# Optimization experiments

Hardware: AMD Instinct MI355X
Metric: run time of the kernel (lower is better)

## Reference

```python
import jax, jax.numpy as jnp
import numpy as np

B, T, C = 2, 2048, 768
H = 12
D = C // H  # head size = 64
F = 4 * C
EPS = 1e-5


def _layernorm(x, g, b):
    mu = jnp.mean(x, axis=-1, keepdims=True)
    var = jnp.var(x, axis=-1, keepdims=True)
    return (x - mu) * jax.lax.rsqrt(var + EPS) * g + b


def setup_inputs() -> dict:
    key = jax.random.key(0)
    ks = jax.random.split(key, 16)
    s_in = 1.0 / np.sqrt(C)
    s_ff = 1.0 / np.sqrt(F)
    return {
        "x": jax.random.normal(ks[0], (B, T, C), dtype=jnp.float32),
        # per-head projection weights, stacked [H, C, D] (no bias, as in nn.Linear(bias=False))
        "Wq": jax.random.uniform(ks[1], (H, C, D), jnp.float32, -s_in, s_in),
        "Wk": jax.random.uniform(ks[2], (H, C, D), jnp.float32, -s_in, s_in),
        "Wv": jax.random.uniform(ks[3], (H, C, D), jnp.float32, -s_in, s_in),
        "Wp": jax.random.uniform(ks[4], (C, C), jnp.float32, -s_in, s_in),
        "bp": jax.random.uniform(ks[5], (C,), jnp.float32, -s_in, s_in),
        "W1": jax.random.uniform(ks[6], (C, F), jnp.float32, -s_in, s_in),
        "b1": jax.random.uniform(ks[7], (F,), jnp.float32, -s_in, s_in),
        "W2": jax.random.uniform(ks[8], (F, C), jnp.float32, -s_ff, s_ff),
        "b2": jax.random.uniform(ks[9], (C,), jnp.float32, -s_ff, s_ff),
        "ln1_g": jnp.ones((C,), jnp.float32),
        "ln1_b": jnp.zeros((C,), jnp.float32),
        "ln2_g": jnp.ones((C,), jnp.float32),
        "ln2_b": jnp.zeros((C,), jnp.float32),
    }


def reference(x, Wq, Wk, Wv, Wp, bp, W1, b1, W2, b2, ln1_g, ln1_b, ln2_g, ln2_b):
    # --- self-attention sublayer (pre-LN) ---
    h = _layernorm(x, ln1_g, ln1_b)                      # [B,T,C]
    q = jnp.einsum('btc,hcd->bhtd', h, Wq)
    k = jnp.einsum('btc,hcd->bhtd', h, Wk)
    v = jnp.einsum('btc,hcd->bhtd', h, Wv)
    # NOTE: original scales by C**-0.5 where C = n_embd (full width), not head size
    scale = C ** (-0.5)
    wei = jnp.einsum('bhtd,bhsd->bhts', q, k) * scale    # [B,H,T,T]
    causal = jnp.tril(jnp.ones((T, T), dtype=bool))
    wei = jnp.where(causal, wei, -jnp.inf)
    wei = jax.nn.softmax(wei, axis=-1)
    out = jnp.einsum('bhts,bhsd->bhtd', wei, v)          # [B,H,T,D]
    out = out.transpose(0, 2, 1, 3).reshape(B, T, C)     # concat heads
    sa = out @ Wp + bp
    x = x + sa
    # --- feed-forward sublayer (pre-LN); ReLU after BOTH linears, as in source ---
    h2 = _layernorm(x, ln2_g, ln2_b)
    ff = jax.nn.relu(jax.nn.relu(h2 @ W1 + b1) @ W2 + b2)
    return x + ff
```

## Files before the change

kernel.cpp:

```cpp
#include <hip/hip_runtime.h>
#include <hip/hip_bf16.h>

#define TSEQ 2048
#define CDIM 768
#define NHEAD 12
#define DHEAD 64
#define FDIM 3072
#define MROWS 4096
#define BH 24

typedef __attribute__((ext_vector_type(8))) short short8;
typedef __attribute__((ext_vector_type(4))) float f32x4;

__device__ inline unsigned short f2bf(float f) {
  __hip_bfloat16 h = __float2bfloat16(f);
  return __builtin_bit_cast(unsigned short, h);
}
__device__ inline float bf2f(unsigned short u) {
  unsigned int v = ((unsigned int)u) << 16;
  return __builtin_bit_cast(float, v);
}

__device__ inline void gload16(const unsigned short* g, unsigned short* l) {
  __builtin_amdgcn_global_load_lds(
      (const __attribute__((address_space(1))) unsigned int*)g,
      (__attribute__((address_space(3))) unsigned int*)l, 16, 0, 0);
}

__global__ __launch_bounds__(256) void prep_all(
    const float* __restrict__ Wq, const float* __restrict__ Wk,
    const float* __restrict__ Wv, const float* __restrict__ Wp,
    const float* __restrict__ W1, const float* __restrict__ W2,
    unsigned short* __restrict__ WqkvT, unsigned short* __restrict__ WpT,
    unsigned short* __restrict__ W1T, unsigned short* __restrict__ W2T,
    const float* __restrict__ x, const float* __restrict__ ln1g,
    const float* __restrict__ ln1b, unsigned short* __restrict__ h1) {
  __shared__ float tile[32][33];
  __shared__ float red[8];
  int b = blockIdx.x;
  if (b >= 6912) {
    int row = b - 6912;
    int tid = threadIdx.x;
    const float* xr = x + (size_t)row * CDIM;
    float v[3];
    float s = 0.f;
#pragma unroll
    for (int i = 0; i < 3; ++i) { v[i] = xr[tid + i * 256]; s += v[i]; }
#pragma unroll
    for (int m = 1; m < 64; m <<= 1) s += __shfl_xor(s, m);
    int w = tid >> 6;
    if ((tid & 63) == 0) red[w] = s;
    __syncthreads();
    float mean = (red[0] + red[1] + red[2] + red[3]) * (1.f / CDIM);
    float vs = 0.f;
#pragma unroll
    for (int i = 0; i < 3; ++i) { float d = v[i] - mean; vs += d * d; }
#pragma unroll
    for (int m = 1; m < 64; m <<= 1) vs += __shfl_xor(vs, m);
    if ((tid & 63) == 0) red[4 + w] = vs;
    __syncthreads();
    float var = (red[4] + red[5] + red[6] + red[7]) * (1.f / CDIM);
    float rstd = rsqrtf(var + 1e-5f);
    unsigned short* orow = h1 + (size_t)row * CDIM;
#pragma unroll
    for (int i = 0; i < 3; ++i) {
      int c = tid + i * 256;
      orow[c] = f2bf((v[i] - mean) * rstd * ln1g[c] + ln1b[c]);
    }
    return;
  }
  int xx = threadIdx.x & 31, y = threadIdx.x >> 5;
  if (b < 1728) {
    int cx = b % 24, dy = (b / 24) % 2, ph = b / 48;
    int proj = ph / NHEAD, h = ph % NHEAD;
    const float* in = (proj == 0 ? Wq : (proj == 1 ? Wk : Wv)) + (size_t)h * CDIM * DHEAD;
    int c0 = cx * 32, d0 = dy * 32;
#pragma unroll
    for (int i = 0; i < 4; ++i)
      tile[y + i * 8][xx] = in[(size_t)(c0 + y + i * 8) * DHEAD + d0 + xx];
    __syncthreads();
#pragma unroll
    for (int i = 0; i < 4; ++i)
      WqkvT[(size_t)(proj * CDIM + h * DHEAD + d0 + y + i * 8) * CDIM + c0 + xx] =
          f2bf(tile[xx][y + i * 8]);
  } else {
    const float* in;
    unsigned short* out;
    int R, C, bx, by;
    if (b < 2304) {
      int b2 = b - 1728;
      in = Wp; out = WpT; R = CDIM; C = CDIM; bx = b2 % 24; by = b2 / 24;
    } else if (b < 4608) {
      int b2 = b - 2304;
      in = W1; out = W1T; R = CDIM; C = FDIM; bx = b2 % 96; by = b2 / 96;
    } else {
      int b2 = b - 4608;
      in = W2; out = W2T; R = FDIM; C = CDIM; bx = b2 % 24; by = b2 / 24;
    }
    int c0 = bx * 32, r0 = by * 32;
#pragma unroll
    for (int i = 0; i < 4; ++i)
      tile[y + i * 8][xx] = in[(size_t)(r0 + y + i * 8) * C + c0 + xx];
    __syncthreads();
#pragma unroll
    for (int i = 0; i < 4; ++i)
      out[(size_t)(c0 + y + i * 8) * R + r0 + xx] = f2bf(tile[xx][y + i * 8]);
  }
}

__global__ __launch_bounds__(256) void ln_kernel(
    const float* __restrict__ x, const float* __restrict__ g,
    const float* __restrict__ b, unsigned short* __restrict__ out) {
  int row = blockIdx.x;
  int tid = threadIdx.x;
  const float* xr = x + (size_t)row * CDIM;
  float v[3];
  float s = 0.f;
#pragma unroll
  for (int i = 0; i < 3; ++i) { v[i] = xr[tid + i * 256]; s += v[i]; }
#pragma unroll
  for (int m = 1; m < 64; m <<= 1) s += __shfl_xor(s, m);
  __shared__ float red[8];
  int w = tid >> 6;
  if ((tid & 63) == 0) red[w] = s;
  __syncthreads();
  float mean = (red[0] + red[1] + red[2] + red[3]) * (1.f / CDIM);
  float vs = 0.f;
#pragma unroll
  for (int i = 0; i < 3; ++i) { float d = v[i] - mean; vs += d * d; }
#pragma unroll
  for (int m = 1; m < 64; m <<= 1) vs += __shfl_xor(vs, m);
  if ((tid & 63) == 0) red[4 + w] = vs;
  __syncthreads();
  float var = (red[4] + red[5] + red[6] + red[7]) * (1.f / CDIM);
  float rstd = rsqrtf(var + 1e-5f);
  unsigned short* orow = out + (size_t)row * CDIM;
#pragma unroll
  for (int i = 0; i < 3; ++i) {
    int c = tid + i * 256;
    orow[c] = f2bf((v[i] - mean) * rstd * g[c] + b[c]);
  }
}

template <int EPI, int SPLITK = 1>
__global__ __launch_bounds__(256) void gemm_bt(
    const unsigned short* __restrict__ A, const unsigned short* __restrict__ BT,
    int M, int N, int K,
    const float* __restrict__ bias, const float* __restrict__ aux,
    float* __restrict__ outf, unsigned short* __restrict__ outb,
    unsigned short* __restrict__ qo, unsigned short* __restrict__ ko,
    unsigned short* __restrict__ vo) {
  __shared__ unsigned short As[128 * 64];
  __shared__ unsigned short Bs[128 * 64];
  int tid = threadIdx.x;
  int lane = tid & 63, wave = tid >> 6;
  int wr = wave >> 1, wc = wave & 1;
  int l15 = lane & 15, lg = lane >> 4;
  int lr = lane >> 3, lc = lane & 7;
  int chunk = gridDim.x >> 3;
  int logical = (blockIdx.x & 7) * chunk + (blockIdx.x >> 3);
  int mt = M >> 7;
  int tiles = mt * (N >> 7);
  int split = logical / tiles;
  int tl = logical % tiles;
  size_t bm = (size_t)(tl % mt) * 128, bn = (size_t)(tl / mt) * 128;
  int Ks = K / SPLITK;
  int kbeg = split * Ks, kend = kbeg + Ks;
  f32x4 acc[4][4] = {};

  for (int kt = kbeg; kt < kend; kt += 64) {
#pragma unroll
    for (int i = 0; i < 4; ++i) {
      int r0 = (wave * 4 + i) * 8;
      gload16(A + (bm + r0 + lr) * K + kt + (lc ^ lr) * 8, &As[r0 * 64]);
      gload16(BT + (bn + r0 + lr) * K + kt + (lc ^ lr) * 8, &Bs[r0 * 64]);
    }
    __syncthreads();
    __builtin_amdgcn_s_setprio(1);
#pragma unroll
    for (int kk = 0; kk < 64; kk += 32) {
      int kb = kk + lg * 8;
      short8 af[4], bfr[4];
#pragma unroll
      for (int m = 0; m < 4; ++m) {
        int row = wr * 64 + m * 16 + l15;
        af[m] = *reinterpret_cast<const short8*>(&As[row * 64 + (kb ^ ((row & 7) << 3))]);
      }
#pragma unroll
      for (int n = 0; n < 4; ++n) {
        int row = wc * 64 + n * 16 + l15;
        bfr[n] = *reinterpret_cast<const short8*>(&Bs[row * 64 + (kb ^ ((row & 7) << 3))]);
      }
#pragma unroll
      for (int m = 0; m < 4; ++m)
#pragma unroll
        for (int n = 0; n < 4; ++n)
          acc[m][n] = __builtin_amdgcn_mfma_f32_16x16x32_bf16(af[m], bfr[n], acc[m][n], 0, 0, 0);
    }
    __builtin_amdgcn_s_setprio(0);
    __syncthreads();
  }

#pragma unroll
  for (int m = 0; m < 4; ++m) {
#pragma unroll
    for (int n = 0; n < 4; ++n) {
#pragma unroll
      for (int r = 0; r < 4; ++r) {
        int row = (int)bm + wr * 64 + m * 16 + lg * 4 + r;
        int col = (int)bn + wc * 64 + n * 16 + l15;
        float val = acc[m][n][r];
        if constexpr (EPI == 0) {
          int proj = col / CDIM, rem = col % CDIM;
          int h = rem >> 6, d = rem & 63;
          int b = row >> 11, t = row & (TSEQ - 1);
          if (proj == 0) {
            qo[(((size_t)(b * NHEAD + h)) * TSEQ + t) * DHEAD + d] =
                f2bf(val * 0.05205877247186126f);
          } else if (proj == 1) {
            ko[(((size_t)(b * NHEAD + h)) * TSEQ + t) * DHEAD + d] = f2bf(val);
          } else {
            vo[(((size_t)(b * NHEAD + h)) * DHEAD + d) * TSEQ + t] = f2bf(val);
          }
        } else if constexpr (EPI == 1) {
          size_t idx = (size_t)row * CDIM + col;
          outf[idx] = val + bias[col] + aux[idx];
        } else if constexpr (EPI == 2) {
          size_t idx = (size_t)row * FDIM + col;
          outb[idx] = f2bf(fmaxf(val + bias[col], 0.f));
        } else if constexpr (EPI == 3) {
          size_t idx = (size_t)row * CDIM + col;
          outf[idx] = aux[idx] + fmaxf(val + bias[col], 0.f);
        } else {
          outb[(size_t)split * M * N + (size_t)row * N + col] = f2bf(val);
        }
      }
    }
  }
}

__global__ __launch_bounds__(256) void ff2_reduce(
    const unsigned short* __restrict__ part,
    const float* __restrict__ bias, const float* __restrict__ x1,
    float* __restrict__ out) {
  int e = (blockIdx.x * 256 + threadIdx.x) * 4;
  int col = e % CDIM;
  float4 xv = *reinterpret_cast<const float4*>(x1 + e);
  float4 bv = *reinterpret_cast<const float4*>(bias + col);
  float s0 = 0.f, s1 = 0.f, s2 = 0.f, s3 = 0.f;
#pragma unroll
  for (int p = 0; p < 4; ++p) {
    short4 pv = *reinterpret_cast<const short4*>(part + (size_t)p * MROWS * CDIM + e);
    s0 += bf2f((unsigned short)pv.x);
    s1 += bf2f((unsigned short)pv.y);
    s2 += bf2f((unsigned short)pv.z);
    s3 += bf2f((unsigned short)pv.w);
  }
  float4 ov;
  ov.x = xv.x + fmaxf(s0 + bv.x, 0.f);
  ov.y = xv.y + fmaxf(s1 + bv.y, 0.f);
  ov.z = xv.z + fmaxf(s2 + bv.z, 0.f);
  ov.w = xv.w + fmaxf(s3 + bv.w, 0.f);
  *reinterpret_cast<float4*>(out + e) = ov;
}

__global__ __launch_bounds__(256) void attn_kernel(
    const unsigned short* __restrict__ Q, const unsigned short* __restrict__ Kd,
    const unsigned short* __restrict__ VT, unsigned short* __restrict__ O) {
  __shared__ unsigned short Kl[3][64 * 64];
  __shared__ unsigned short Vl[3][64 * 64];
  __shared__ unsigned short plds[4][16 * 64];
  int tid = threadIdx.x;
  int wave = tid >> 6, lane = tid & 63;
  int l15 = lane & 15, lg = lane >> 4;
  int bid = blockIdx.x;
  int xcd = bid & 7, idx = bid >> 3;
  int bh = xcd * 3 + idx / 16;
  int p = idx & 15;
  const unsigned short* qp = Q + (size_t)bh * TSEQ * DHEAD;
  const unsigned short* kp = Kd + (size_t)bh * TSEQ * DHEAD;
  const unsigned short* vp = VT + (size_t)bh * DHEAD * TSEQ;
  unsigned short* pw = plds[wave];
  int b = bh / NHEAD, h = bh % NHEAD;

  short8 ones;
  {
    unsigned short ov = (l15 == 0) ? (unsigned short)0x3F80 : (unsigned short)0;
#pragma unroll
    for (int j = 0; j < 8; ++j) ones[j] = (short)ov;
  }

  int lr = lane >> 3, lc = lane & 7;
  int jsw = lc ^ lr;

  auto stage = [&](int t, int buf) {
    int s0 = t * 64;
#pragma unroll
    for (int i = 0; i < 2; ++i) {
      int r0 = (wave * 2 + i) * 8;
      gload16(kp + (size_t)(s0 + r0 + lr) * DHEAD + jsw * 8, &Kl[buf][r0 * 64]);
      gload16(vp + (size_t)(r0 + lr) * TSEQ + s0 + jsw * 8, &Vl[buf][r0 * 64]);
    }
  };

  auto run_stripe = [&](int stripe) {
    int qbase = stripe * 64 + wave * 16;
    int nt = stripe + 1;
    short8 qf[2];
#pragma unroll
    for (int kk = 0; kk < 2; ++kk)
      qf[kk] = *reinterpret_cast<const short8*>(
          qp + (size_t)(qbase + l15) * DHEAD + kk * 32 + lg * 8);
    f32x4 oacc[5] = {};

    stage(0, 0);
    if (nt > 1) {
      stage(1, 1);
      asm volatile("s_waitcnt vmcnt(4)" ::: "memory");
    } else {
      asm volatile("s_waitcnt vmcnt(0)" ::: "memory");
    }
    __builtin_amdgcn_s_barrier();

    for (int t = 0; t < nt; ++t) {
      int cur = t % 3;
      bool pre2 = (t + 2 < nt);
      if (pre2) stage(t + 2, (t + 2) % 3);
      int s0 = t * 64;
      f32x4 sacc[4] = {};
      __builtin_amdgcn_s_setprio(1);
#pragma unroll
      for (int st = 0; st < 4; ++st) {
        int row = st * 16 + l15;
        int sw = row & 7;
#pragma unroll
        for (int kk = 0; kk < 2; ++kk) {
          short8 kf = *reinterpret_cast<const short8*>(
              &Kl[cur][row * 64 + (((kk * 4 + lg) ^ sw) * 8)]);
          sacc[st] = __builtin_amdgcn_mfma_f32_16x16x32_bf16(qf[kk], kf, sacc[st], 0, 0, 0);
        }
      }
      __builtin_amdgcn_s_setprio(0);
      bool last = (t == nt - 1);
#pragma unroll
      for (int r = 0; r < 4; ++r) {
        int qrow = qbase + lg * 4 + r;
        int prow = lg * 4 + r;
        int psw = (prow & 7) << 3;
        if (last) {
#pragma unroll
          for (int st = 0; st < 4; ++st) {
            float pv = exp2f(sacc[st][r]);
            if (s0 + st * 16 + l15 > qrow) pv = 0.f;
            pw[prow * 64 + ((st * 16 + l15) ^ psw)] = f2bf(pv);
          }
        } else {
#pragma unroll
          for (int st = 0; st < 4; ++st)
            pw[prow * 64 + ((st * 16 + l15) ^ psw)] = f2bf(exp2f(sacc[st][r]));
        }
      }
      int prsw = (l15 & 7) << 3;
      short8 pa0 = *reinterpret_cast<const short8*>(&pw[l15 * 64 + ((lg * 8) ^ prsw)]);
      short8 pa1 = *reinterpret_cast<const short8*>(&pw[l15 * 64 + ((32 + lg * 8) ^ prsw)]);
      __builtin_amdgcn_s_setprio(1);
#pragma unroll
      for (int n = 0; n < 4; ++n) {
        int row = n * 16 + l15;
        int sw = row & 7;
        short8 vf0 = *reinterpret_cast<const short8*>(&Vl[cur][row * 64 + ((lg ^ sw) * 8)]);
        oacc[n] = __builtin_amdgcn_mfma_f32_16x16x32_bf16(pa0, vf0, oacc[n], 0, 0, 0);
        short8 vf1 = *reinterpret_cast<const short8*>(&Vl[cur][row * 64 + (((4 + lg) ^ sw) * 8)]);
        oacc[n] = __builtin_amdgcn_mfma_f32_16x16x32_bf16(pa1, vf1, oacc[n], 0, 0, 0);
      }
      oacc[4] = __builtin_amdgcn_mfma_f32_16x16x32_bf16(pa0, ones, oacc[4], 0, 0, 0);
      oacc[4] = __builtin_amdgcn_mfma_f32_16x16x32_bf16(pa1, ones, oacc[4], 0, 0, 0);
      __builtin_amdgcn_s_setprio(0);
      if (pre2) asm volatile("s_waitcnt vmcnt(4)" ::: "memory");
      else      asm volatile("s_waitcnt vmcnt(0)" ::: "memory");
      __builtin_amdgcn_s_barrier();
    }

#pragma unroll
    for (int r = 0; r < 4; ++r) {
      float lsum = __shfl(oacc[4][r], lane & 48);
      float inv = 1.f / lsum;
      int row = qbase + lg * 4 + r;
#pragma unroll
      for (int n = 0; n < 4; ++n)
        O[(size_t)(b * TSEQ + row) * CDIM + h * DHEAD + n * 16 + l15] =
            f2bf(oacc[n][r] * inv);
    }
  };

  run_stripe(31 - p);
  run_stripe(p);
}

extern "C" void kernel_launch(void* const* d_in, const int* in_sizes, int n_in,
                              void* d_out, int out_size, void* d_ws, size_t ws_size,
                              hipStream_t stream) {
  const float* x    = (const float*)d_in[0];
  const float* Wq   = (const float*)d_in[1];
  const float* Wk   = (const float*)d_in[2];
  const float* Wv   = (const float*)d_in[3];
  const float* Wp   = (const float*)d_in[4];
  const float* bp   = (const float*)d_in[5];
  const float* W1   = (const float*)d_in[6];
  const float* b1   = (const float*)d_in[7];
  const float* W2   = (const float*)d_in[8];
  const float* b2   = (const float*)d_in[9];
  const float* ln1g = (const float*)d_in[10];
  const float* ln1b = (const float*)d_in[11];
  const float* ln2g = (const float*)d_in[12];
  const float* ln2b = (const float*)d_in[13];
  float* out = (float*)d_out;

  char* ws = (char*)d_ws;
  auto alloc = [&](size_t bytes) {
    char* p = ws;
    ws += (bytes + 255) & ~(size_t)255;
    return p;
  };
  unsigned short* h1    = (unsigned short*)alloc((size_t)MROWS * CDIM * 2);
  unsigned short* WqkvT = (unsigned short*)alloc((size_t)3 * CDIM * CDIM * 2);
  unsigned short* WpT   = (unsigned short*)alloc((size_t)CDIM * CDIM * 2);
  unsigned short* W1T   = (unsigned short*)alloc((size_t)FDIM * CDIM * 2);
  unsigned short* W2T   = (unsigned short*)alloc((size_t)CDIM * FDIM * 2);
  unsigned short* Qb    = (unsigned short*)alloc((size_t)BH * TSEQ * DHEAD * 2);
  unsigned short* Kb    = (unsigned short*)alloc((size_t)BH * TSEQ * DHEAD * 2);
  unsigned short* VTb   = (unsigned short*)alloc((size_t)BH * TSEQ * DHEAD * 2);
  unsigned short* AO    = (unsigned short*)alloc((size_t)MROWS * CDIM * 2);
  float*          x1    = (float*)alloc((size_t)MROWS * CDIM * 4);
  unsigned short* h2    = (unsigned short*)alloc((size_t)MROWS * CDIM * 2);
  unsigned short* a1    = (unsigned short*)alloc((size_t)MROWS * FDIM * 2);
  unsigned short* partF = Qb;

  prep_all<<<11008, 256, 0, stream>>>(Wq, Wk, Wv, Wp, W1, W2,
                                      WqkvT, WpT, W1T, W2T, x, ln1g, ln1b, h1);
  gemm_bt<0><<<576, 256, 0, stream>>>(h1, WqkvT, MROWS, 3 * CDIM, CDIM,
                                      nullptr, nullptr, nullptr, nullptr, Qb, Kb, VTb);
  attn_kernel<<<384, 256, 0, stream>>>(Qb, Kb, VTb, AO);
  gemm_bt<1><<<192, 256, 0, stream>>>(AO, WpT, MROWS, CDIM, CDIM,
                                      bp, x, x1, nullptr, nullptr, nullptr, nullptr);
  ln_kernel<<<4096, 256, 0, stream>>>(x1, ln2g, ln2b, h2);
  gemm_bt<2><<<768, 256, 0, stream>>>(h2, W1T, MROWS, FDIM, CDIM,
                                      b1, nullptr, nullptr, a1, nullptr, nullptr, nullptr);
  gemm_bt<4, 4><<<768, 256, 0, stream>>>(a1, W2T, MROWS, CDIM, FDIM,
                                         nullptr, nullptr, nullptr, partF,
                                         nullptr, nullptr, nullptr);
  ff2_reduce<<<3072, 256, 0, stream>>>(partF, b2, x1, out);
}
```

Before: 194.8 us.

## Stage V tile through LDS for coalesced transposed stores; split-K the output projection

The QKV GEMM epilogue now writes the V tiles into padded shared memory transposed and then emits 16-byte coalesced stores into the V^T layout, replacing scattered 2-byte strided stores. The output projection GEMM moves from 192 blocks with a fused residual epilogue to split-K=2 with 384 blocks, writing bf16 partials that a new templated reduce kernel sums with bias and residual. This targets the uncoalesced V write and the low occupancy of the small projection GEMM. The cost is an extra kernel launch, an extra round trip of partials through memory, and bf16 rounding of the partial sums.

```diff
diff --git a/kernel.cpp b/kernel.cpp
--- a/kernel.cpp
+++ b/kernel.cpp
@@ -150,8 +150,10 @@
     float* __restrict__ outf, unsigned short* __restrict__ outb,
     unsigned short* __restrict__ qo, unsigned short* __restrict__ ko,
     unsigned short* __restrict__ vo) {
-  __shared__ unsigned short As[128 * 64];
-  __shared__ unsigned short Bs[128 * 64];
+  constexpr int SH_CNT = (EPI == 0) ? 128 * 136 : 2 * 128 * 64;
+  __shared__ unsigned short sh[SH_CNT];
+  unsigned short* As = sh;
+  unsigned short* Bs = sh + 128 * 64;
   int tid = threadIdx.x;
   int lane = tid & 63, wave = tid >> 6;
   int wr = wave >> 1, wc = wave & 1;
@@ -201,55 +203,93 @@
     __syncthreads();
   }
 
-#pragma unroll
-  for (int m = 0; m < 4; ++m) {
-#pragma unroll
-    for (int n = 0; n < 4; ++n) {
-#pragma unroll
-      for (int r = 0; r < 4; ++r) {
-        int row = (int)bm + wr * 64 + m * 16 + lg * 4 + r;
-        int col = (int)bn + wc * 64 + n * 16 + l15;
-        float val = acc[m][n][r];
-        if constexpr (EPI == 0) {
-          int proj = col / CDIM, rem = col % CDIM;
-          int h = rem >> 6, d = rem & 63;
-          int b = row >> 11, t = row & (TSEQ - 1);
-          if (proj == 0) {
-            qo[(((size_t)(b * NHEAD + h)) * TSEQ + t) * DHEAD + d] =
-                f2bf(val * 0.05205877247186126f);
-          } else if (proj == 1) {
-            ko[(((size_t)(b * NHEAD + h)) * TSEQ + t) * DHEAD + d] = f2bf(val);
+  if constexpr (EPI == 0) {
+    if (bn >= 1536) {
+#pragma unroll
+      for (int m = 0; m < 4; ++m)
+#pragma unroll
+        for (int n = 0; n < 4; ++n)
+#pragma unroll
+          for (int r = 0; r < 4; ++r) {
+            int rowL = wr * 64 + m * 16 + lg * 4 + r;
+            int c = wc * 64 + n * 16 + l15;
+            sh[c * 136 + rowL] = f2bf(acc[m][n][r]);
+          }
+      __syncthreads();
+      int bb = (int)(bm >> 11);
+      int t0g = (int)(bm & 2047);
+      int vbase = (int)bn - 1536;
+#pragma unroll
+      for (int it = 0; it < 8; ++it) {
+        int ch = it * 256 + tid;
+        int c = ch >> 4, tlc = (ch & 15) * 8;
+        int vcol = vbase + c;
+        int hh = vcol >> 6, dd = vcol & 63;
+        *reinterpret_cast<int4*>(
+            vo + (((size_t)(bb * NHEAD + hh)) * DHEAD + dd) * TSEQ + t0g + tlc) =
+            *reinterpret_cast<const int4*>(&sh[c * 136 + tlc]);
+      }
+    } else {
+#pragma unroll
+      for (int m = 0; m < 4; ++m)
+#pragma unroll
+        for (int n = 0; n < 4; ++n)
+#pragma unroll
+          for (int r = 0; r < 4; ++r) {
+            int row = (int)bm + wr * 64 + m * 16 + lg * 4 + r;
+            int col = (int)bn + wc * 64 + n * 16 + l15;
+            float val = acc[m][n][r];
+            int proj = col / CDIM, rem = col % CDIM;
+            int h = rem >> 6, d = rem & 63;
+            int b = row >> 11, t = row & (TSEQ - 1);
+            if (proj == 0) {
+              qo[(((size_t)(b * NHEAD + h)) * TSEQ + t) * DHEAD + d] =
+                  f2bf(val * 0.05205877247186126f);
+            } else {
+              ko[(((size_t)(b * NHEAD + h)) * TSEQ + t) * DHEAD + d] = f2bf(val);
+            }
+          }
+    }
+  } else {
+#pragma unroll
+    for (int m = 0; m < 4; ++m) {
+#pragma unroll
+      for (int n = 0; n < 4; ++n) {
+#pragma unroll
+        for (int r = 0; r < 4; ++r) {
+          int row = (int)bm + wr * 64 + m * 16 + lg * 4 + r;
+          int col = (int)bn + wc * 64 + n * 16 + l15;
+          float val = acc[m][n][r];
+          if constexpr (EPI == 1) {
+            size_t idx = (size_t)row * CDIM + col;
+            outf[idx] = val + bias[col] + aux[idx];
+          } else if constexpr (EPI == 2) {
+            size_t idx = (size_t)row * FDIM + col;
+            outb[idx] = f2bf(fmaxf(val + bias[col], 0.f));
+          } else if constexpr (EPI == 3) {
+            size_t idx = (size_t)row * CDIM + col;
+            outf[idx] = aux[idx] + fmaxf(val + bias[col], 0.f);
           } else {
-            vo[(((size_t)(b * NHEAD + h)) * DHEAD + d) * TSEQ + t] = f2bf(val);
+            outb[(size_t)split * M * N + (size_t)row * N + col] = f2bf(val);
           }
-        } else if constexpr (EPI == 1) {
-          size_t idx = (size_t)row * CDIM + col;
-          outf[idx] = val + bias[col] + aux[idx];
-        } else if constexpr (EPI == 2) {
-          size_t idx = (size_t)row * FDIM + col;
-          outb[idx] = f2bf(fmaxf(val + bias[col], 0.f));
-        } else if constexpr (EPI == 3) {
-          size_t idx = (size_t)row * CDIM + col;
-          outf[idx] = aux[idx] + fmaxf(val + bias[col], 0.f);
-        } else {
-          outb[(size_t)split * M * N + (size_t)row * N + col] = f2bf(val);
         }
       }
     }
   }
 }
 
-__global__ __launch_bounds__(256) void ff2_reduce(
+template <int NPART, bool RELU>
+__global__ __launch_bounds__(256) void reduce_k(
     const unsigned short* __restrict__ part,
-    const float* __restrict__ bias, const float* __restrict__ x1,
+    const float* __restrict__ bias, const float* __restrict__ aux,
     float* __restrict__ out) {
   int e = (blockIdx.x * 256 + threadIdx.x) * 4;
   int col = e % CDIM;
-  float4 xv = *reinterpret_cast<const float4*>(x1 + e);
+  float4 xv = *reinterpret_cast<const float4*>(aux + e);
   float4 bv = *reinterpret_cast<const float4*>(bias + col);
   float s0 = 0.f, s1 = 0.f, s2 = 0.f, s3 = 0.f;
 #pragma unroll
-  for (int p = 0; p < 4; ++p) {
+  for (int p = 0; p < NPART; ++p) {
     short4 pv = *reinterpret_cast<const short4*>(part + (size_t)p * MROWS * CDIM + e);
     s0 += bf2f((unsigned short)pv.x);
     s1 += bf2f((unsigned short)pv.y);
@@ -257,10 +297,17 @@
     s3 += bf2f((unsigned short)pv.w);
   }
   float4 ov;
-  ov.x = xv.x + fmaxf(s0 + bv.x, 0.f);
-  ov.y = xv.y + fmaxf(s1 + bv.y, 0.f);
-  ov.z = xv.z + fmaxf(s2 + bv.z, 0.f);
-  ov.w = xv.w + fmaxf(s3 + bv.w, 0.f);
+  if constexpr (RELU) {
+    ov.x = xv.x + fmaxf(s0 + bv.x, 0.f);
+    ov.y = xv.y + fmaxf(s1 + bv.y, 0.f);
+    ov.z = xv.z + fmaxf(s2 + bv.z, 0.f);
+    ov.w = xv.w + fmaxf(s3 + bv.w, 0.f);
+  } else {
+    ov.x = xv.x + s0 + bv.x;
+    ov.y = xv.y + s1 + bv.y;
+    ov.z = xv.z + s2 + bv.z;
+    ov.w = xv.w + s3 + bv.w;
+  }
   *reinterpret_cast<float4*>(out + e) = ov;
 }
 
@@ -434,20 +481,22 @@
   float*          x1    = (float*)alloc((size_t)MROWS * CDIM * 4);
   unsigned short* h2    = (unsigned short*)alloc((size_t)MROWS * CDIM * 2);
   unsigned short* a1    = (unsigned short*)alloc((size_t)MROWS * FDIM * 2);
-  unsigned short* partF = Qb;
+  unsigned short* partP = Qb;
 
   prep_all<<<11008, 256, 0, stream>>>(Wq, Wk, Wv, Wp, W1, W2,
                                       WqkvT, WpT, W1T, W2T, x, ln1g, ln1b, h1);
   gemm_bt<0><<<576, 256, 0, stream>>>(h1, WqkvT, MROWS, 3 * CDIM, CDIM,
                                       nullptr, nullptr, nullptr, nullptr, Qb, Kb, VTb);
   attn_kernel<<<384, 256, 0, stream>>>(Qb, Kb, VTb, AO);
-  gemm_bt<1><<<192, 256, 0, stream>>>(AO, WpT, MROWS, CDIM, CDIM,
-                                      bp, x, x1, nullptr, nullptr, nullptr, nullptr);
+  gemm_bt<4, 2><<<384, 256, 0, stream>>>(AO, WpT, MROWS, CDIM, CDIM,
+                                         nullptr, nullptr, nullptr, partP,
+                                         nullptr, nullptr, nullptr);
+  reduce_k<2, false><<<3072, 256, 0, stream>>>(partP, bp, x, x1);
   ln_kernel<<<4096, 256, 0, stream>>>(x1, ln2g, ln2b, h2);
   gemm_bt<2><<<768, 256, 0, stream>>>(h2, W1T, MROWS, FDIM, CDIM,
                                       b1, nullptr, nullptr, a1, nullptr, nullptr, nullptr);
   gemm_bt<4, 4><<<768, 256, 0, stream>>>(a1, W2T, MROWS, CDIM, FDIM,
-                                         nullptr, nullptr, nullptr, partF,
+                                         nullptr, nullptr, nullptr, partP,
                                          nullptr, nullptr, nullptr);
-  ff2_reduce<<<3072, 256, 0, stream>>>(partF, b2, x1, out);
-}
+  reduce_k<4, true><<<3072, 256, 0, stream>>>(partP, b2, x1, out);
+}
```

Result: faster. 164.2 us (-15.7%).
